# Kernel optimization log

Measured on AMD Instinct MI355X. Metric: run time of the kernel, lower is better.

The kernel has to match this reference:

```python
import jax, jax.numpy as jnp
import numpy as np

N = 100000
E = 3200000
IN = 128
HID = 128   # 2 * out_channels
OUT = 64


def setup_inputs() -> dict:
    key = jax.random.key(0)
    ks = jax.random.split(key, 8)
    x = jax.random.normal(ks[0], (N, IN), dtype=jnp.float32)
    edge_index = jax.random.randint(ks[1], (2, E), 0, N, dtype=jnp.int64)
    s1 = 1.0 / np.sqrt(IN)
    s2 = 1.0 / np.sqrt(HID)
    # PyG GraphConv per layer: lin_rel (with bias) applied to aggregated neighbors,
    # lin_root (no bias) applied to the node itself. Linear weight is (out, in).
    W1_rel = jax.random.uniform(ks[2], (HID, IN), jnp.float32, -s1, s1)
    b1 = jax.random.uniform(ks[3], (HID,), jnp.float32, -s1, s1)
    W1_root = jax.random.uniform(ks[4], (HID, IN), jnp.float32, -s1, s1)
    W2_rel = jax.random.uniform(ks[5], (OUT, HID), jnp.float32, -s2, s2)
    b2 = jax.random.uniform(ks[6], (OUT,), jnp.float32, -s2, s2)
    W2_root = jax.random.uniform(ks[7], (OUT, HID), jnp.float32, -s2, s2)
    return {"x": x, "edge_index": edge_index, "W1_rel": W1_rel, "b1": b1,
            "W1_root": W1_root, "W2_rel": W2_rel, "b2": b2, "W2_root": W2_root}


def _graph_conv(h, src, dst, W_rel, b, W_root, num_nodes):
    # sum-aggregate neighbor features at dst, then affine combine with root term
    agg = jax.ops.segment_sum(h[src], dst, num_segments=num_nodes)  # [N, d_in]
    return agg @ W_rel.T + b + h @ W_root.T


def reference(x, edge_index, W1_rel, b1, W1_root, W2_rel, b2, W2_root):
    src = edge_index[0]
    dst = edge_index[1]
    n = x.shape[0]
    h = _graph_conv(x, src, dst, W1_rel, b1, W1_root, n)
    h = jax.nn.relu(h)  # dropout p=0.0 -> identity
    return _graph_conv(h, src, dst, W2_rel, b2, W2_root, n)
```

## Files before the change

kernel.cpp:

```cpp
#include <hip/hip_runtime.h>
#include <hip/hip_bf16.h>


#define EB 8192
#define NB_MAX 512

typedef __attribute__((ext_vector_type(8))) short bf16x8;
typedef __attribute__((ext_vector_type(4))) float f32x4;
typedef __attribute__((ext_vector_type(2))) float f32x2;

__device__ __forceinline__ uint pack_bf16x2(float a, float b) {
    __hip_bfloat162 p = __float22bfloat162_rn(make_float2(a, b));
    return *(uint*)&p;
}

__device__ __forceinline__ uchar pack_fp8(float v) {
    uint p = __builtin_amdgcn_cvt_pk_fp8_f32(v, v, 0, false);
    return (uchar)(p & 0xff);
}

__device__ __forceinline__ float bflo(uint g) { return __uint_as_float(g << 16); }
__device__ __forceinline__ float bfhi(uint g) { return __uint_as_float(g & 0xffff0000u); }


__global__ __launch_bounds__(256) void bucket_hist(const int* __restrict__ dst, int E,
                                                   int NB, int* __restrict__ hist) {
    __shared__ int h[NB_MAX];
    int t = threadIdx.x;
    for (int i = t; i < NB; i += 256) h[i] = 0;
    __syncthreads();
    int e0 = blockIdx.x * EB, e1 = min(E, e0 + EB);
    for (int e = e0 + t; e < e1; e += 256) atomicAdd(&h[dst[e] >> 8], 1);
    __syncthreads();
    int* row = hist + (size_t)blockIdx.x * NB;
    for (int i = t; i < NB; i += 256) row[i] = h[i];
}

__global__ __launch_bounds__(256) void scan_blocks(int* __restrict__ hist, int NBLK,
                                                   int NB, int* __restrict__ total) {
    __shared__ int s[256];
    __shared__ int carry;
    int b = blockIdx.x, t = threadIdx.x;
    if (t == 0) carry = 0;
    __syncthreads();
    for (int start = 0; start < NBLK; start += 256) {
        int i = start + t;
        int v = (i < NBLK) ? hist[(size_t)i * NB + b] : 0;
        s[t] = v;
        __syncthreads();
        for (int off = 1; off < 256; off <<= 1) {
            int u = (t >= off) ? s[t - off] : 0;
            __syncthreads();
            s[t] += u;
            __syncthreads();
        }
        if (i < NBLK) hist[(size_t)i * NB + b] = carry + s[t] - v;
        __syncthreads();
        if (t == 255) carry += s[255];
        __syncthreads();
    }
    if (t == 0) total[b] = carry;
}

__global__ __launch_bounds__(512) void scan_total(const int* __restrict__ total, int NB,
                                                  int* __restrict__ base) {
    __shared__ int s[512];
    int t = threadIdx.x;
    int v = (t < NB) ? total[t] : 0;
    s[t] = v;
    __syncthreads();
    for (int off = 1; off < 512; off <<= 1) {
        int u = (t >= off) ? s[t - off] : 0;
        __syncthreads();
        s[t] += u;
        __syncthreads();
    }
    if (t < NB) base[t] = s[t] - v;
}

__global__ __launch_bounds__(256) void bucket_scatter(const int* __restrict__ src,
                                                      const int* __restrict__ dst, int E,
                                                      int NB, const int* __restrict__ hist,
                                                      const int* __restrict__ base,
                                                      uint* __restrict__ ebuf) {
    __shared__ int cur[NB_MAX];
    int t = threadIdx.x, blk = blockIdx.x;
    const int* row = hist + (size_t)blk * NB;
    for (int i = t; i < NB; i += 256) cur[i] = base[i] + row[i];
    __syncthreads();
    int e0 = blk * EB, e1 = min(E, e0 + EB);
    for (int e = e0 + t; e < e1; e += 256) {
        int d = dst[e];
        int p = atomicAdd(&cur[d >> 8], 1);
        ebuf[p] = ((uint)(d & 255) << 24) | (uint)src[e];
    }
}

__global__ __launch_bounds__(256) void build_csr_bucket(const uint* __restrict__ ebuf,
                                                        const int* __restrict__ base,
                                                        const int* __restrict__ total,
                                                        int NB, int N, int E,
                                                        int* __restrict__ rowptr,
                                                        int* __restrict__ col) {
    __shared__ int cnt[256];
    __shared__ int s[256];
    __shared__ int cur[256];
    int b = blockIdx.x, t = threadIdx.x;
    int e0 = base[b], e1 = e0 + total[b];
    cnt[t] = 0;
    __syncthreads();
    for (int e = e0 + t; e < e1; e += 256) atomicAdd(&cnt[ebuf[e] >> 24], 1);
    __syncthreads();
    int v = cnt[t];
    s[t] = v;
    __syncthreads();
    for (int off = 1; off < 256; off <<= 1) {
        int u = (t >= off) ? s[t - off] : 0;
        __syncthreads();
        s[t] += u;
        __syncthreads();
    }
    int start = e0 + s[t] - v;
    int node = (b << 8) + t;
    if (node < N) rowptr[node] = start;
    if (b == NB - 1 && t == 0) rowptr[N] = E;
    cur[t] = start;
    __syncthreads();
    for (int e = e0 + t; e < e1; e += 256) {
        uint ev = ebuf[e];
        int p = atomicAdd(&cur[ev >> 24], 1);
        col[p] = (int)(ev & 0xFFFFFFu);
    }
}


#define LDK 72

template <int C, bool A_BF16, bool Y_FP8>
__global__ __launch_bounds__(256, 2) void gemm_mfma(const void* __restrict__ Aptr,
                                                    const float* __restrict__ Wa,
                                                    const float* __restrict__ Wb,
                                                    const float* __restrict__ bias,
                                                    void* __restrict__ Yout,
                                                    float* __restrict__ Z, int n_rows) {
    __shared__ ushort Xs[128 * LDK];
    __shared__ ushort Ws[128 * LDK];

    const int t = threadIdx.x;
    const int lane = t & 63;
    const int wave = t >> 6;
    const int wm = wave >> 1, wn = wave & 1;
    const int row0 = blockIdx.x * 128;
    const int tn = blockIdx.y;
    const int fr = lane & 15;
    const int quad = lane >> 4;

    f32x4 acc[4][4];
#pragma unroll
    for (int i = 0; i < 4; i++)
#pragma unroll
        for (int j = 0; j < 4; j++) acc[i][j] = (f32x4){0.f, 0.f, 0.f, 0.f};

    for (int ko = 0; ko < 2; ++ko) {
        if (A_BF16) {
            const ushort* A = (const ushort*)Aptr;
#pragma unroll
            for (int j = 0; j < 4; ++j) {
                int f = j * 256 + t;
                int r = f >> 3, c = f & 7;
                int grow = row0 + r;
                uint4 v = make_uint4(0u, 0u, 0u, 0u);
                if (grow < n_rows)
                    v = *(const uint4*)(A + (size_t)grow * 128 + ko * 64 + c * 8);
                *(uint4*)(&Xs[r * LDK + c * 8]) = v;
            }
        } else {
            const float* A = (const float*)Aptr;
#pragma unroll
            for (int j = 0; j < 8; ++j) {
                int f = j * 256 + t;
                int r = f >> 4, c = f & 15;
                int grow = row0 + r;
                float4 v = make_float4(0.f, 0.f, 0.f, 0.f);
                if (grow < n_rows)
                    v = *(const float4*)(A + (size_t)grow * 128 + ko * 64 + c * 4);
                uint2 u;
                u.x = pack_bf16x2(v.x, v.y);
                u.y = pack_bf16x2(v.z, v.w);
                *(uint2*)(&Xs[r * LDK + c * 4]) = u;
            }
        }
#pragma unroll
        for (int j = 0; j < 8; ++j) {
            int f = j * 256 + t;
            int r = f >> 4, c = f & 15;
            int grow = tn * 128 + r;
            const float* Wr = (grow < C) ? (Wa + (size_t)grow * 128)
                                         : (Wb + (size_t)(grow - C) * 128);
            float4 v = *(const float4*)(Wr + ko * 64 + c * 4);
            uint2 u;
            u.x = pack_bf16x2(v.x, v.y);
            u.y = pack_bf16x2(v.z, v.w);
            *(uint2*)(&Ws[r * LDK + c * 4]) = u;
        }
        __syncthreads();

#pragma unroll
        for (int ks = 0; ks < 2; ++ks) {
            bf16x8 a[4], b[4];
#pragma unroll
            for (int mt = 0; mt < 4; ++mt)
                a[mt] = *(const bf16x8*)(&Xs[(wm * 64 + mt * 16 + fr) * LDK +
                                             ks * 32 + quad * 8]);
#pragma unroll
            for (int nt = 0; nt < 4; ++nt)
                b[nt] = *(const bf16x8*)(&Ws[(wn * 64 + nt * 16 + fr) * LDK +
                                             ks * 32 + quad * 8]);
#pragma unroll
            for (int mt = 0; mt < 4; ++mt)
#pragma unroll
                for (int nt = 0; nt < 4; ++nt)
                    acc[mt][nt] = __builtin_amdgcn_mfma_f32_16x16x32_bf16(
                        a[mt], b[nt], acc[mt][nt], 0, 0, 0);
        }
        __syncthreads();
    }

#pragma unroll
    for (int nt = 0; nt < 4; ++nt) {
        int gcol = tn * 128 + wn * 64 + nt * 16 + fr;
        if (gcol < C) {
#pragma unroll
            for (int mt = 0; mt < 4; ++mt) {
#pragma unroll
                for (int r = 0; r < 4; ++r) {
                    int grow = row0 + wm * 64 + mt * 16 + quad * 4 + r;
                    if (grow < n_rows) {
                        if (Y_FP8) {
                            ((uchar*)Yout)[(size_t)grow * C + gcol] =
                                pack_fp8(acc[mt][nt][r]);
                        } else {
                            __hip_bfloat16 hb = __float2bfloat16(acc[mt][nt][r]);
                            ((ushort*)Yout)[(size_t)grow * C + gcol] = *(ushort*)&hb;
                        }
                    }
                }
            }
        } else {
            float bv = bias[gcol - C];
#pragma unroll
            for (int mt = 0; mt < 4; ++mt) {
#pragma unroll
                for (int r = 0; r < 4; ++r) {
                    int grow = row0 + wm * 64 + mt * 16 + quad * 4 + r;
                    if (grow < n_rows)
                        Z[(size_t)grow * C + (gcol - C)] = acc[mt][nt][r] + bv;
                }
            }
        }
    }
}


__global__ __launch_bounds__(256) void agg_relu_l1(const uchar* __restrict__ Y1,
                                                   const float* __restrict__ Z1,
                                                   const int* __restrict__ rowptr,
                                                   const int* __restrict__ col,
                                                   ushort* __restrict__ h, int n_nodes) {
    int node = (blockIdx.x * 256 + threadIdx.x) >> 6;
    if (node >= n_nodes) return;
    int lane = threadIdx.x & 63;
    int sub = lane >> 3;
    int cg  = lane & 7;
    int beg = rowptr[node], end = rowptr[node + 1];
    float acc[16];
#pragma unroll
    for (int i = 0; i < 16; i++) acc[i] = 0.f;

    int e = beg;
    for (; e + 16 <= end; e += 16) {
        int s0 = col[e + sub];
        int s1 = col[e + 8 + sub];
        uint4 v0 = *(const uint4*)(Y1 + (size_t)s0 * 128 + cg * 16);
        uint4 v1 = *(const uint4*)(Y1 + (size_t)s1 * 128 + cg * 16);
        f32x2 p;
        p = __builtin_amdgcn_cvt_pk_f32_fp8(v0.x, false); acc[0] += p[0]; acc[1] += p[1];
        p = __builtin_amdgcn_cvt_pk_f32_fp8(v0.x, true);  acc[2] += p[0]; acc[3] += p[1];
        p = __builtin_amdgcn_cvt_pk_f32_fp8(v0.y, false); acc[4] += p[0]; acc[5] += p[1];
        p = __builtin_amdgcn_cvt_pk_f32_fp8(v0.y, true);  acc[6] += p[0]; acc[7] += p[1];
        p = __builtin_amdgcn_cvt_pk_f32_fp8(v0.z, false); acc[8] += p[0]; acc[9] += p[1];
        p = __builtin_amdgcn_cvt_pk_f32_fp8(v0.z, true);  acc[10] += p[0]; acc[11] += p[1];
        p = __builtin_amdgcn_cvt_pk_f32_fp8(v0.w, false); acc[12] += p[0]; acc[13] += p[1];
        p = __builtin_amdgcn_cvt_pk_f32_fp8(v0.w, true);  acc[14] += p[0]; acc[15] += p[1];
        p = __builtin_amdgcn_cvt_pk_f32_fp8(v1.x, false); acc[0] += p[0]; acc[1] += p[1];
        p = __builtin_amdgcn_cvt_pk_f32_fp8(v1.x, true);  acc[2] += p[0]; acc[3] += p[1];
        p = __builtin_amdgcn_cvt_pk_f32_fp8(v1.y, false); acc[4] += p[0]; acc[5] += p[1];
        p = __builtin_amdgcn_cvt_pk_f32_fp8(v1.y, true);  acc[6] += p[0]; acc[7] += p[1];
        p = __builtin_amdgcn_cvt_pk_f32_fp8(v1.z, false); acc[8] += p[0]; acc[9] += p[1];
        p = __builtin_amdgcn_cvt_pk_f32_fp8(v1.z, true);  acc[10] += p[0]; acc[11] += p[1];
        p = __builtin_amdgcn_cvt_pk_f32_fp8(v1.w, false); acc[12] += p[0]; acc[13] += p[1];
        p = __builtin_amdgcn_cvt_pk_f32_fp8(v1.w, true);  acc[14] += p[0]; acc[15] += p[1];
    }
    for (; e < end; e += 8) {
        int ee = e + sub;
        uint4 v = make_uint4(0u, 0u, 0u, 0u);
        if (ee < end)
            v = *(const uint4*)(Y1 + (size_t)col[ee] * 128 + cg * 16);
        f32x2 p;
        p = __builtin_amdgcn_cvt_pk_f32_fp8(v.x, false); acc[0] += p[0]; acc[1] += p[1];
        p = __builtin_amdgcn_cvt_pk_f32_fp8(v.x, true);  acc[2] += p[0]; acc[3] += p[1];
        p = __builtin_amdgcn_cvt_pk_f32_fp8(v.y, false); acc[4] += p[0]; acc[5] += p[1];
        p = __builtin_amdgcn_cvt_pk_f32_fp8(v.y, true);  acc[6] += p[0]; acc[7] += p[1];
        p = __builtin_amdgcn_cvt_pk_f32_fp8(v.z, false); acc[8] += p[0]; acc[9] += p[1];
        p = __builtin_amdgcn_cvt_pk_f32_fp8(v.z, true);  acc[10] += p[0]; acc[11] += p[1];
        p = __builtin_amdgcn_cvt_pk_f32_fp8(v.w, false); acc[12] += p[0]; acc[13] += p[1];
        p = __builtin_amdgcn_cvt_pk_f32_fp8(v.w, true);  acc[14] += p[0]; acc[15] += p[1];
    }

#pragma unroll
    for (int off = 8; off < 64; off <<= 1)
#pragma unroll
        for (int i = 0; i < 16; i++) acc[i] += __shfl_xor(acc[i], off, 64);

    if (sub == 0) {
        const float4* zp = (const float4*)(Z1 + (size_t)node * 128 + cg * 16);
        uint o[8];
#pragma unroll
        for (int q = 0; q < 4; ++q) {
            float4 z = zp[q];
            float r0 = acc[q * 4 + 0] + z.x;
            float r1 = acc[q * 4 + 1] + z.y;
            float r2 = acc[q * 4 + 2] + z.z;
            float r3 = acc[q * 4 + 3] + z.w;
            r0 = r0 > 0.f ? r0 : 0.f;
            r1 = r1 > 0.f ? r1 : 0.f;
            r2 = r2 > 0.f ? r2 : 0.f;
            r3 = r3 > 0.f ? r3 : 0.f;
            o[q * 2 + 0] = pack_bf16x2(r0, r1);
            o[q * 2 + 1] = pack_bf16x2(r2, r3);
        }
        uint* hp = (uint*)(h + (size_t)node * 128) + cg * 8;
        *(uint4*)(hp + 0) = make_uint4(o[0], o[1], o[2], o[3]);
        *(uint4*)(hp + 4) = make_uint4(o[4], o[5], o[6], o[7]);
    }
}


__global__ __launch_bounds__(256) void agg_l2(const ushort* __restrict__ Y2,
                                              const float* __restrict__ Z2,
                                              const int* __restrict__ rowptr,
                                              const int* __restrict__ col,
                                              float* __restrict__ out, int n_nodes) {
    int node = (blockIdx.x * 256 + threadIdx.x) >> 6;
    if (node >= n_nodes) return;
    int lane = threadIdx.x & 63;
    int sub = lane >> 3;
    int cg  = lane & 7;
    int beg = rowptr[node], end = rowptr[node + 1];
    float acc[8];
#pragma unroll
    for (int i = 0; i < 8; i++) acc[i] = 0.f;

    int e = beg;
    for (; e + 16 <= end; e += 16) {
        int s0 = col[e + sub];
        int s1 = col[e + 8 + sub];
        uint4 v0 = *(const uint4*)(Y2 + (size_t)s0 * 64 + cg * 8);
        uint4 v1 = *(const uint4*)(Y2 + (size_t)s1 * 64 + cg * 8);
        acc[0] += bflo(v0.x) + bflo(v1.x);
        acc[1] += bfhi(v0.x) + bfhi(v1.x);
        acc[2] += bflo(v0.y) + bflo(v1.y);
        acc[3] += bfhi(v0.y) + bfhi(v1.y);
        acc[4] += bflo(v0.z) + bflo(v1.z);
        acc[5] += bfhi(v0.z) + bfhi(v1.z);
        acc[6] += bflo(v0.w) + bflo(v1.w);
        acc[7] += bfhi(v0.w) + bfhi(v1.w);
    }
    for (; e < end; e += 8) {
        int ee = e + sub;
        uint4 v = make_uint4(0u, 0u, 0u, 0u);
        if (ee < end)
            v = *(const uint4*)(Y2 + (size_t)col[ee] * 64 + cg * 8);
        acc[0] += bflo(v.x);
        acc[1] += bfhi(v.x);
        acc[2] += bflo(v.y);
        acc[3] += bfhi(v.y);
        acc[4] += bflo(v.z);
        acc[5] += bfhi(v.z);
        acc[6] += bflo(v.w);
        acc[7] += bfhi(v.w);
    }

#pragma unroll
    for (int off = 8; off < 64; off <<= 1)
#pragma unroll
        for (int i = 0; i < 8; i++) acc[i] += __shfl_xor(acc[i], off, 64);

    if (sub == 0) {
        const float4* zp = (const float4*)(Z2 + (size_t)node * 64 + cg * 8);
        float4 z0 = zp[0], z1 = zp[1];
        float4 o0 = {acc[0] + z0.x, acc[1] + z0.y, acc[2] + z0.z, acc[3] + z0.w};
        float4 o1 = {acc[4] + z1.x, acc[5] + z1.y, acc[6] + z1.z, acc[7] + z1.w};
        float4* op = (float4*)(out + (size_t)node * 64 + cg * 8);
        op[0] = o0;
        op[1] = o1;
    }
}


extern "C" void kernel_launch(void* const* d_in, const int* in_sizes, int n_in,
                              void* d_out, int out_size, void* d_ws, size_t ws_size,
                              hipStream_t stream) {
    const float* x       = (const float*)d_in[0];
    const int*   ei      = (const int*)d_in[1];
    const float* W1_rel  = (const float*)d_in[2];
    const float* b1      = (const float*)d_in[3];
    const float* W1_root = (const float*)d_in[4];
    const float* W2_rel  = (const float*)d_in[5];
    const float* b2      = (const float*)d_in[6];
    const float* W2_root = (const float*)d_in[7];
    float* out = (float*)d_out;

    const int N = in_sizes[0] / 128;
    const int E = in_sizes[1] / 2;
    const int* srcA = ei;
    const int* dstA = ei + E;
    const int NB   = (N + 255) >> 8;
    const int NBLK = (E + EB - 1) / EB;

    char* ws = (char*)d_ws;
    size_t cur = 0;
    auto alloc = [&](size_t bytes) -> void* {
        size_t o = cur;
        cur = (cur + bytes + 511) & ~(size_t)511;
        return (void*)(ws + o);
    };
    uchar*  Y1  = (uchar*)alloc((size_t)N * 128);
    float*  Z1  = (float*)alloc((size_t)N * 128 * 4);
    ushort* h   = (ushort*)alloc((size_t)N * 128 * 2);
    ushort* Y2  = (ushort*)alloc((size_t)N * 64 * 2);
    float*  Z2  = (float*)alloc((size_t)N * 64 * 4);
    int* rowptr = (int*)alloc((size_t)(N + 1) * 4);
    int* colA   = (int*)alloc((size_t)E * 4);
    int* hist   = (int*)alloc((size_t)NBLK * NB * 4);
    int* btotal = (int*)alloc((size_t)NB_MAX * 4);
    int* bbase  = (int*)alloc((size_t)NB_MAX * 4);
    uint* ebuf  = (uint*)h;

    bucket_hist<<<NBLK, 256, 0, stream>>>(dstA, E, NB, hist);
    scan_blocks<<<NB, 256, 0, stream>>>(hist, NBLK, NB, btotal);
    scan_total<<<1, 512, 0, stream>>>(btotal, NB, bbase);
    bucket_scatter<<<NBLK, 256, 0, stream>>>(srcA, dstA, E, NB, hist, bbase, ebuf);
    build_csr_bucket<<<NB, 256, 0, stream>>>(ebuf, bbase, btotal, NB, N, E, rowptr, colA);

    const int gblk = (N + 127) / 128;
    gemm_mfma<128, false, true><<<dim3(gblk, 2), 256, 0, stream>>>(
        x, W1_rel, W1_root, b1, Y1, Z1, N);
    agg_relu_l1<<<(N + 3) / 4, 256, 0, stream>>>(Y1, Z1, rowptr, colA, h, N);
    gemm_mfma<64, true, false><<<dim3(gblk, 1), 256, 0, stream>>>(
        h, W2_rel, W2_root, b2, Y2, Z2, N);
    agg_l2<<<(N + 3) / 4, 256, 0, stream>>>(Y2, Z2, rowptr, colA, out, N);
}
```

Before: 426.1 us.

## Load GEMM operands directly from global memory and pre-convert weights to bf16

A small prep kernel now converts both layers' weight matrices to bf16 once per call. The GEMM drops its shared-memory staging and barriers: each wave loads its A and B MFMA fragments straight from global memory (converting x from fp32 inline) and relies on cache for reuse. Occupancy is raised to 3 blocks per CU. This removes LDS traffic and syncs, but each fragment is now re-read from L1/L2 by several waves with less coalesced access.

After: 408.1 us. 1.04x faster.

```diff
diff --git a/kernel.cpp b/kernel.cpp
--- a/kernel.cpp
+++ b/kernel.cpp
@@ -134,18 +134,43 @@
 }
 
 
-#define LDK 72
+__global__ __launch_bounds__(256) void prep_w(const float* __restrict__ W1_rel,
+                                              const float* __restrict__ W1_root,
+                                              const float* __restrict__ W2_rel,
+                                              const float* __restrict__ W2_root,
+                                              ushort* __restrict__ Wb1,
+                                              ushort* __restrict__ Wb2) {
+    int t = blockIdx.x * 256 + threadIdx.x;
+    if (t < 8192) {
+        int idx = t * 4;
+        int row = idx >> 7, c = idx & 127;
+        const float* src = (row < 128) ? W1_rel + (size_t)row * 128 + c
+                                       : W1_root + (size_t)(row - 128) * 128 + c;
+        float4 v = *(const float4*)src;
+        uint2 u;
+        u.x = pack_bf16x2(v.x, v.y);
+        u.y = pack_bf16x2(v.z, v.w);
+        *(uint2*)(Wb1 + idx) = u;
+    } else if (t < 12288) {
+        int idx = (t - 8192) * 4;
+        int row = idx >> 7, c = idx & 127;
+        const float* src = (row < 64) ? W2_rel + (size_t)row * 128 + c
+                                      : W2_root + (size_t)(row - 64) * 128 + c;
+        float4 v = *(const float4*)src;
+        uint2 u;
+        u.x = pack_bf16x2(v.x, v.y);
+        u.y = pack_bf16x2(v.z, v.w);
+        *(uint2*)(Wb2 + idx) = u;
+    }
+}
+
 
 template <int C, bool A_BF16, bool Y_FP8>
-__global__ __launch_bounds__(256, 2) void gemm_mfma(const void* __restrict__ Aptr,
-                                                    const float* __restrict__ Wa,
-                                                    const float* __restrict__ Wb,
-                                                    const float* __restrict__ bias,
-                                                    void* __restrict__ Yout,
-                                                    float* __restrict__ Z, int n_rows) {
-    __shared__ ushort Xs[128 * LDK];
-    __shared__ ushort Ws[128 * LDK];
-
+__global__ __launch_bounds__(256, 3) void gemm_direct(const void* __restrict__ Aptr,
+                                                      const ushort* __restrict__ Wb16,
+                                                      const float* __restrict__ bias,
+                                                      void* __restrict__ Yout,
+                                                      float* __restrict__ Z, int n_rows) {
     const int t = threadIdx.x;
     const int lane = t & 63;
     const int wave = t >> 6;
@@ -161,69 +186,43 @@
 #pragma unroll
         for (int j = 0; j < 4; j++) acc[i][j] = (f32x4){0.f, 0.f, 0.f, 0.f};
 
-    for (int ko = 0; ko < 2; ++ko) {
-        if (A_BF16) {
-            const ushort* A = (const ushort*)Aptr;
-#pragma unroll
-            for (int j = 0; j < 4; ++j) {
-                int f = j * 256 + t;
-                int r = f >> 3, c = f & 7;
-                int grow = row0 + r;
-                uint4 v = make_uint4(0u, 0u, 0u, 0u);
-                if (grow < n_rows)
-                    v = *(const uint4*)(A + (size_t)grow * 128 + ko * 64 + c * 8);
-                *(uint4*)(&Xs[r * LDK + c * 8]) = v;
-            }
-        } else {
-            const float* A = (const float*)Aptr;
-#pragma unroll
-            for (int j = 0; j < 8; ++j) {
-                int f = j * 256 + t;
-                int r = f >> 4, c = f & 15;
-                int grow = row0 + r;
-                float4 v = make_float4(0.f, 0.f, 0.f, 0.f);
-                if (grow < n_rows)
-                    v = *(const float4*)(A + (size_t)grow * 128 + ko * 64 + c * 4);
-                uint2 u;
-                u.x = pack_bf16x2(v.x, v.y);
-                u.y = pack_bf16x2(v.z, v.w);
-                *(uint2*)(&Xs[r * LDK + c * 4]) = u;
+    int ar[4];
+#pragma unroll
+    for (int mt = 0; mt < 4; ++mt) {
+        int r = row0 + wm * 64 + mt * 16 + fr;
+        ar[mt] = (r < n_rows) ? r : (n_rows - 1);
+    }
+    const int brbase = tn * 128 + wn * 64;
+
+#pragma unroll
+    for (int kk = 0; kk < 4; ++kk) {
+        const int kb = kk * 32 + quad * 8;
+        bf16x8 a[4], b[4];
+#pragma unroll
+        for (int mt = 0; mt < 4; ++mt) {
+            if (A_BF16) {
+                a[mt] = *(const bf16x8*)((const ushort*)Aptr + (size_t)ar[mt] * 128 + kb);
+            } else {
+                const float* p = (const float*)Aptr + (size_t)ar[mt] * 128 + kb;
+                float4 v0 = *(const float4*)p;
+                float4 v1 = *(const float4*)(p + 4);
+                uint4 u;
+                u.x = pack_bf16x2(v0.x, v0.y);
+                u.y = pack_bf16x2(v0.z, v0.w);
+                u.z = pack_bf16x2(v1.x, v1.y);
+                u.w = pack_bf16x2(v1.z, v1.w);
+                a[mt] = *(bf16x8*)&u;
             }
         }
 #pragma unroll
-        for (int j = 0; j < 8; ++j) {
-            int f = j * 256 + t;
-            int r = f >> 4, c = f & 15;
-            int grow = tn * 128 + r;
-            const float* Wr = (grow < C) ? (Wa + (size_t)grow * 128)
-                                         : (Wb + (size_t)(grow - C) * 128);
-            float4 v = *(const float4*)(Wr + ko * 64 + c * 4);
-            uint2 u;
-            u.x = pack_bf16x2(v.x, v.y);
-            u.y = pack_bf16x2(v.z, v.w);
-            *(uint2*)(&Ws[r * LDK + c * 4]) = u;
-        }
-        __syncthreads();
-
-#pragma unroll
-        for (int ks = 0; ks < 2; ++ks) {
-            bf16x8 a[4], b[4];
-#pragma unroll
-            for (int mt = 0; mt < 4; ++mt)
-                a[mt] = *(const bf16x8*)(&Xs[(wm * 64 + mt * 16 + fr) * LDK +
-                                             ks * 32 + quad * 8]);
+        for (int nt = 0; nt < 4; ++nt)
+            b[nt] = *(const bf16x8*)(Wb16 + (size_t)(brbase + nt * 16 + fr) * 128 + kb);
+#pragma unroll
+        for (int mt = 0; mt < 4; ++mt)
 #pragma unroll
             for (int nt = 0; nt < 4; ++nt)
-                b[nt] = *(const bf16x8*)(&Ws[(wn * 64 + nt * 16 + fr) * LDK +
-                                             ks * 32 + quad * 8]);
-#pragma unroll
-            for (int mt = 0; mt < 4; ++mt)
-#pragma unroll
-                for (int nt = 0; nt < 4; ++nt)
-                    acc[mt][nt] = __builtin_amdgcn_mfma_f32_16x16x32_bf16(
-                        a[mt], b[nt], acc[mt][nt], 0, 0, 0);
-        }
-        __syncthreads();
+                acc[mt][nt] = __builtin_amdgcn_mfma_f32_16x16x32_bf16(
+                    a[mt], b[nt], acc[mt][nt], 0, 0, 0);
     }
 
 #pragma unroll
@@ -445,7 +444,11 @@
     int* hist   = (int*)alloc((size_t)NBLK * NB * 4);
     int* btotal = (int*)alloc((size_t)NB_MAX * 4);
     int* bbase  = (int*)alloc((size_t)NB_MAX * 4);
+    ushort* Wb1 = (ushort*)alloc((size_t)256 * 128 * 2);
+    ushort* Wb2 = (ushort*)alloc((size_t)128 * 128 * 2);
     uint* ebuf  = (uint*)h;
+
+    prep_w<<<48, 256, 0, stream>>>(W1_rel, W1_root, W2_rel, W2_root, Wb1, Wb2);
 
     bucket_hist<<<NBLK, 256, 0, stream>>>(dstA, E, NB, hist);
     scan_blocks<<<NB, 256, 0, stream>>>(hist, NBLK, NB, btotal);
@@ -454,10 +457,10 @@
     build_csr_bucket<<<NB, 256, 0, stream>>>(ebuf, bbase, btotal, NB, N, E, rowptr, colA);
 
     const int gblk = (N + 127) / 128;
-    gemm_mfma<128, false, true><<<dim3(gblk, 2), 256, 0, stream>>>(
-        x, W1_rel, W1_root, b1, Y1, Z1, N);
+    gemm_direct<128, false, true><<<dim3(gblk, 2), 256, 0, stream>>>(
+        x, Wb1, b1, Y1, Z1, N);
     agg_relu_l1<<<(N + 3) / 4, 256, 0, stream>>>(Y1, Z1, rowptr, colA, h, N);
-    gemm_mfma<64, true, false><<<dim3(gblk, 1), 256, 0, stream>>>(
-        h, W2_rel, W2_root, b2, Y2, Z2, N);
+    gemm_direct<64, true, false><<<dim3(gblk, 1), 256, 0, stream>>>(
+        h, Wb2, b2, Y2, Z2, N);
     agg_l2<<<(N + 3) / 4, 256, 0, stream>>>(Y2, Z2, rowptr, colA, out, N);
 }
```
